# Kernel optimization log

Hardware: AMD Instinct MI355X
Metric: run time of the kernel (lower is better)

The kernel has to match this reference:

```python
import jax, jax.numpy as jnp
import numpy as np

# Fixed-point fake-quant config: Q8.8 (int_bits=8, frac_bits=8, 16-bit signed total)
INT_BITS = 8
FRAC_BITS = 8
SCALE = 2.0 ** FRAC_BITS
QMIN = float(-(2 ** (INT_BITS + FRAC_BITS - 1)))
QMAX = float(2 ** (INT_BITS + FRAC_BITS - 1) - 1)


def fpq(x):
    # round-to-nearest, clamp to signed Q8.8 range, rescale; straight-through estimator
    q = jnp.clip(jnp.round(x * SCALE), QMIN, QMAX) / SCALE
    return x + jax.lax.stop_gradient(q - x)


def qconv2d(x, w, b):
    # stride 1, padding 1, 3x3 kernel -> SAME spatial size
    y = jax.lax.conv_general_dilated(
        x, w, window_strides=(1, 1), padding=((1, 1), (1, 1)),
        dimension_numbers=("NCHW", "OIHW", "NCHW"))
    return fpq(y + b[None, :, None, None])


def qmaxpool2(x):
    y = jax.lax.reduce_window(x, -jnp.inf, jax.lax.max,
                              window_dimensions=(1, 1, 2, 2),
                              window_strides=(1, 1, 2, 2), padding="VALID")
    return fpq(y)


def qlinear(x, w, b):
    return fpq(x @ w.T + b)


def setup_inputs() -> dict:
    key = jax.random.key(0)
    ks = jax.random.split(key, 9)
    B = 4096
    x = jax.random.normal(ks[0], (B, 1, 28, 28), dtype=jnp.float32)
    conv1_w = jax.random.normal(ks[1], (16, 1, 3, 3), dtype=jnp.float32) * 0.1
    conv1_b = jax.random.normal(ks[2], (16,), dtype=jnp.float32) * 0.01
    conv2_w = jax.random.normal(ks[3], (32, 16, 3, 3), dtype=jnp.float32) * 0.05
    conv2_b = jax.random.normal(ks[4], (32,), dtype=jnp.float32) * 0.01
    fc1_w = jax.random.normal(ks[5], (128, 32 * 7 * 7), dtype=jnp.float32) * 0.02
    fc1_b = jax.random.normal(ks[6], (128,), dtype=jnp.float32) * 0.01
    fc2_w = jax.random.normal(ks[7], (10, 128), dtype=jnp.float32) * 0.05
    fc2_b = jax.random.normal(ks[8], (10,), dtype=jnp.float32) * 0.01
    return {"x": x, "conv1_w": conv1_w, "conv1_b": conv1_b,
            "conv2_w": conv2_w, "conv2_b": conv2_b,
            "fc1_w": fc1_w, "fc1_b": fc1_b, "fc2_w": fc2_w, "fc2_b": fc2_b}


def reference(x, conv1_w, conv1_b, conv2_w, conv2_b, fc1_w, fc1_b, fc2_w, fc2_b):
    h = jax.nn.relu(qconv2d(x, conv1_w, conv1_b))          # [B,16,28,28]
    h = qmaxpool2(h)                                        # [B,16,14,14]
    h = jax.nn.relu(qconv2d(h, conv2_w, conv2_b))          # [B,32,14,14]
    h = qmaxpool2(h)                                        # [B,32,7,7]
    h = h.reshape(h.shape[0], 32 * 7 * 7)
    h = jax.nn.relu(qlinear(h, fc1_w, fc1_b))              # [B,128]
    return qlinear(h, fc2_w, fc2_b)                        # [B,10]
```

## Files before the change

kernel.cpp:

```cpp
#include <hip/hip_runtime.h>

typedef _Float16 half4 __attribute__((ext_vector_type(4)));
typedef float f32x4 __attribute__((ext_vector_type(4)));

__global__ void prep_kernel(const float* __restrict__ w1, const float* __restrict__ b1,
                            const float* __restrict__ w2, const float* __restrict__ b2,
                            const float* __restrict__ f1w, const float* __restrict__ f1b,
                            _Float16* __restrict__ wsB, _Float16* __restrict__ wsF,
                            float* __restrict__ w1s, float* __restrict__ b1s,
                            float* __restrict__ b2s, float* __restrict__ b1fs) {
    int i = blockIdx.x * 256 + threadIdx.x;
    if (i < 144) w1s[i]  = __fmul_rn(w1[i], 256.0f);
    if (i < 16)  b1s[i]  = __fmul_rn(b1[i], 256.0f);
    if (i < 32)  b2s[i]  = __fmul_rn(b2[i], 256.0f);
    if (i < 128) b1fs[i] = __fmul_rn(f1b[i], 256.0f);
    if (i < 9216) {
        int ntile = i / 4608, r = i - ntile * 4608;
        int tap = r / 512;  int r2 = r - tap * 512;
        int split = r2 / 256; int lidx = r2 - split * 256;
        int lane = lidx >> 2, j = lidx & 3;
        int ic = ((lane >> 4) << 2) + j;
        int oc = ntile * 16 + (lane & 15);
        float w = w2[oc * 144 + ic * 9 + tap];
        _Float16 wh = (_Float16)w;
        wsB[i] = split ? (_Float16)(w - (float)wh) : wh;
    }
    if (i < 401408) {
        int c = i / 4096, rem = i - c * 4096;
        int sp = rem / 2048; int r2 = rem - sp * 2048;
        int nt = r2 / 256; int lidx = r2 - nt * 256;
        int lane = lidx >> 2, j = lidx & 3;
        int k = c * 16 + ((lane >> 4) << 2) + j;
        int o = nt * 16 + (lane & 15);
        float w = f1w[(size_t)o * 1568 + k];
        _Float16 wh = (_Float16)w;
        wsF[i] = sp ? (_Float16)(w - (float)wh) : wh;
    }
}

#define ICGS 1168

__global__ __launch_bounds__(256) void conv_kernel(
    const float* __restrict__ x,
    const float* __restrict__ w1s, const float* __restrict__ b1s,
    const _Float16* __restrict__ wsB, const float* __restrict__ b2s,
    short* __restrict__ h2s)
{
    __shared__ __align__(16) float    xs[900];
    __shared__ __align__(16) _Float16 h1h[4 * ICGS];
    __shared__ __align__(16) short    c2s[6272];

    const int t = threadIdx.x;
    const int s = blockIdx.x;
    const int lane = t & 63;
    const int wid = t >> 6;

    for (int i = t; i < 900; i += 256) xs[i] = 0.0f;
    for (int i = t; i < 4 * ICGS; i += 256) h1h[i] = (_Float16)0.0f;
    __syncthreads();

    const float* xin = x + (size_t)s * 784;
    for (int i = t; i < 784; i += 256) {
        int r = i / 28, c = i - r * 28;
        xs[(r + 1) * 30 + c + 1] = xin[i];
    }
    __syncthreads();

    {
        const int p  = (t < 196) ? t : 195;
        const int py = p / 14, px = p - 14 * (p / 14);
        const int r0 = 2 * py, c0 = 2 * px;
        float patch[16];
        #pragma unroll
        for (int i = 0; i < 4; ++i)
            #pragma unroll
            for (int j = 0; j < 4; ++j)
                patch[i * 4 + j] = xs[(r0 + i) * 30 + c0 + j];
        #pragma unroll 1
        for (int oc = 0; oc < 16; ++oc) {
            float a0 = 0.f, a1 = 0.f, a2 = 0.f, a3 = 0.f;
            #pragma unroll
            for (int ky = 0; ky < 3; ++ky)
                #pragma unroll
                for (int kx = 0; kx < 3; ++kx) {
                    float w = w1s[oc * 9 + ky * 3 + kx];
                    a0 = __fmaf_rn(patch[ky * 4 + kx],           w, a0);
                    a1 = __fmaf_rn(patch[ky * 4 + kx + 1],       w, a1);
                    a2 = __fmaf_rn(patch[(ky + 1) * 4 + kx],     w, a2);
                    a3 = __fmaf_rn(patch[(ky + 1) * 4 + kx + 1], w, a3);
                }
            float bb = b1s[oc];
            float q0 = rintf(__fadd_rn(a0, bb));
            float q1 = rintf(__fadd_rn(a1, bb));
            float q2 = rintf(__fadd_rn(a2, bb));
            float q3 = rintf(__fadd_rn(a3, bb));
            float m = fmaxf(fmaxf(fmaxf(q0, q1), fmaxf(q2, q3)), 0.f);
            if (t < 196)
                h1h[(oc >> 2) * ICGS + ((py + 1) * 18 + (px + 1)) * 4 + (oc & 3)] = (_Float16)m;
        }
    }
    __syncthreads();

    const half4* __restrict__ wsB4 = (const half4*)wsB;
    for (int nt = 0; nt < 2; ++nt) {
        half4 bh[9], bl[9];
        #pragma unroll
        for (int tap = 0; tap < 9; ++tap) {
            bh[tap] = wsB4[(size_t)((nt * 9 + tap) * 2 + 0) * 64 + lane];
            bl[tap] = wsB4[(size_t)((nt * 9 + tap) * 2 + 1) * 64 + lane];
        }
        const float bb = b2s[nt * 16 + (lane & 15)];
        for (int mt = wid; mt < 13; mt += 4) {
            int p = mt * 16 + (lane & 15);
            p = (p < 196) ? p : 195;
            const int y = p / 14, xx = p - 14 * (p / 14);
            const _Float16* abase = h1h + (lane >> 4) * ICGS + (y * 18 + xx) * 4;

            f32x4 acc = {0.f, 0.f, 0.f, 0.f};
            #pragma unroll
            for (int tap = 0; tap < 9; ++tap) {
                const int aoff = ((tap / 3) * 18 + (tap % 3)) * 4;
                half4 a = *(const half4*)(abase + aoff);
                acc = __builtin_amdgcn_mfma_f32_16x16x16f16(a, bh[tap], acc, 0, 0, 0);
                acc = __builtin_amdgcn_mfma_f32_16x16x16f16(a, bl[tap], acc, 0, 0, 0);
            }
            const int oc = nt * 16 + (lane & 15);
            const int pix0 = mt * 16 + (lane >> 4) * 4;
            #pragma unroll
            for (int j = 0; j < 4; ++j) {
                float qv = fmaxf(rintf(__fadd_rn(acc[j], bb)), 0.f);
                int pix = pix0 + j;
                if (pix < 196) c2s[oc * 196 + pix] = (short)(int)qv;
            }
        }
    }
    __syncthreads();

    short* h2o = h2s + (size_t)s * 1568;
    for (int i = t; i < 1568; i += 256) {
        int oc = i / 49, q = i - oc * 49;
        int qy = q / 7, qx = q - 7 * (q / 7);
        const short* b = c2s + oc * 196 + qy * 28 + qx * 2;
        int m = max(max((int)b[0], (int)b[1]), max((int)b[14], (int)b[15]));
        h2o[i] = (short)m;
    }
}

__global__ __launch_bounds__(256) void fc_kernel(
    const short* __restrict__ h2s,
    const _Float16* __restrict__ wsF, const float* __restrict__ b1fs,
    const float* __restrict__ w2f, const float* __restrict__ b2f,
    float* __restrict__ out)
{
    __shared__ __align__(16) _Float16 Ash[16 * 393 * 4];
    __shared__ short Fsm[16 * 132];

    const int t = threadIdx.x;
    const int s0 = blockIdx.x * 16;
    const int lane = t & 63;
    const int wid = t >> 6;

    for (int i = t; i < 3136; i += 256) {
        int r = i / 196, c = i - r * 196;
        int4 v = *(const int4*)(h2s + (size_t)(s0 + r) * 1568 + c * 8);
        half4 lo, hi;
        lo[0] = (_Float16)(float)(short)(v.x & 0xffff); lo[1] = (_Float16)(float)(short)(v.x >> 16);
        lo[2] = (_Float16)(float)(short)(v.y & 0xffff); lo[3] = (_Float16)(float)(short)(v.y >> 16);
        hi[0] = (_Float16)(float)(short)(v.z & 0xffff); hi[1] = (_Float16)(float)(short)(v.z >> 16);
        hi[2] = (_Float16)(float)(short)(v.w & 0xffff); hi[3] = (_Float16)(float)(short)(v.w >> 16);
        *(half4*)(Ash + (r * 393 + c * 2) * 4)     = lo;
        *(half4*)(Ash + (r * 393 + c * 2 + 1) * 4) = hi;
    }
    __syncthreads();

    const int nt0 = wid * 2, nt1 = wid * 2 + 1;
    const half4* __restrict__ wsF4 = (const half4*)wsF;
    f32x4 acc0 = {0.f, 0.f, 0.f, 0.f};
    f32x4 acc1 = {0.f, 0.f, 0.f, 0.f};

    for (int c = 0; c < 98; ++c) {
        const int kg = c * 4 + (lane >> 4);
        half4 a = *(const half4*)(Ash + ((lane & 15) * 393 + kg) * 4);
        const size_t base = (size_t)(c * 2) * 512 + lane;
        half4 b0h = wsF4[base + (size_t)nt0 * 64];
        half4 b0l = wsF4[base + 512 + (size_t)nt0 * 64];
        half4 b1h = wsF4[base + (size_t)nt1 * 64];
        half4 b1l = wsF4[base + 512 + (size_t)nt1 * 64];
        acc0 = __builtin_amdgcn_mfma_f32_16x16x16f16(a, b0h, acc0, 0, 0, 0);
        acc0 = __builtin_amdgcn_mfma_f32_16x16x16f16(a, b0l, acc0, 0, 0, 0);
        acc1 = __builtin_amdgcn_mfma_f32_16x16x16f16(a, b1h, acc1, 0, 0, 0);
        acc1 = __builtin_amdgcn_mfma_f32_16x16x16f16(a, b1l, acc1, 0, 0, 0);
    }

    {
        const float bb0 = b1fs[nt0 * 16 + (lane & 15)];
        const float bb1 = b1fs[nt1 * 16 + (lane & 15)];
        const int rbase = (lane >> 4) * 4;
        #pragma unroll
        for (int j = 0; j < 4; ++j) {
            float q0 = fmaxf(rintf(__fadd_rn(acc0[j], bb0)), 0.f);
            float q1 = fmaxf(rintf(__fadd_rn(acc1[j], bb1)), 0.f);
            Fsm[(rbase + j) * 132 + nt0 * 16 + (lane & 15)] = (short)(int)q0;
            Fsm[(rbase + j) * 132 + nt1 * 16 + (lane & 15)] = (short)(int)q1;
        }
    }
    __syncthreads();

    if (t < 160) {
        int r = t / 10, c = t - 10 * (t / 10);
        const float* wr = w2f + c * 128;
        double acc = 0.0;
        #pragma unroll 8
        for (int k = 0; k < 128; ++k)
            acc = fma((double)Fsm[r * 132 + k], (double)wr[k], acc);
        out[(size_t)(s0 + r) * 10 + c] = (float)(acc * 0.00390625 + (double)b2f[c]);
    }
}

extern "C" void kernel_launch(void* const* d_in, const int* in_sizes, int n_in,
                              void* d_out, int out_size, void* d_ws, size_t ws_size,
                              hipStream_t stream) {
    const float* x   = (const float*)d_in[0];
    const float* c1w = (const float*)d_in[1];
    const float* c1b = (const float*)d_in[2];
    const float* c2w = (const float*)d_in[3];
    const float* c2b = (const float*)d_in[4];
    const float* f1w = (const float*)d_in[5];
    const float* f1b = (const float*)d_in[6];
    const float* f2w = (const float*)d_in[7];
    const float* f2b = (const float*)d_in[8];
    float* out = (float*)d_out;

    const int B = in_sizes[0] / 784;

    _Float16* wsB = (_Float16*)d_ws;
    _Float16* wsF = wsB + 9216;
    float* fbase  = (float*)(wsF + 401408);
    float* w1s  = fbase;
    float* b1s  = w1s + 144;
    float* b2s  = b1s + 16;
    float* b1fs = b2s + 32;
    short* h2s  = (short*)(b1fs + 128);

    prep_kernel<<<1568, 256, 0, stream>>>(c1w, c1b, c2w, c2b, f1w, f1b,
                                          wsB, wsF, w1s, b1s, b2s, b1fs);
    conv_kernel<<<B, 256, 0, stream>>>(x, w1s, b1s, wsB, b2s, h2s);
    fc_kernel<<<B / 16, 256, 0, stream>>>(h2s, wsF, b1fs, f2w, f2b, out);
}
```

Measured before the change: 82.26 us.

## Split FC into per-N-tile fc1 and separate fc2; fold horizontal pooling into conv epilogue

The conv kernel now max-pools horizontally in the MFMA epilogue, writing a half-size LDS buffer that is unioned with the input tile, and stores pooled activations as fp16. The single fc kernel is split in two. In fc1, each block handles one 16-column output tile, each wave covers 16 samples, and the A operand is read directly from global memory without LDS staging. fc2 is a separate per-output kernel running in double precision. The aim is more parallelism in the FC stage, less LDS use and lower occupancy pressure in conv, and no per-block conversion pass. In exchange it adds a kernel launch and an intermediate global buffer, and fc1 re-reads activations once per N tile.

```diff
diff --git a/kernel.cpp b/kernel.cpp
--- a/kernel.cpp
+++ b/kernel.cpp
@@ -44,25 +44,27 @@
     const float* __restrict__ x,
     const float* __restrict__ w1s, const float* __restrict__ b1s,
     const _Float16* __restrict__ wsB, const float* __restrict__ b2s,
-    short* __restrict__ h2s)
+    _Float16* __restrict__ h2h)
 {
-    __shared__ __align__(16) float    xs[900];
+    __shared__ __align__(16) union {
+        float xs[900];
+        short c2h[32 * 98];
+    } u;
     __shared__ __align__(16) _Float16 h1h[4 * ICGS];
-    __shared__ __align__(16) short    c2s[6272];
 
     const int t = threadIdx.x;
     const int s = blockIdx.x;
     const int lane = t & 63;
     const int wid = t >> 6;
 
-    for (int i = t; i < 900; i += 256) xs[i] = 0.0f;
+    for (int i = t; i < 900; i += 256) u.xs[i] = 0.0f;
     for (int i = t; i < 4 * ICGS; i += 256) h1h[i] = (_Float16)0.0f;
     __syncthreads();
 
     const float* xin = x + (size_t)s * 784;
     for (int i = t; i < 784; i += 256) {
         int r = i / 28, c = i - r * 28;
-        xs[(r + 1) * 30 + c + 1] = xin[i];
+        u.xs[(r + 1) * 30 + c + 1] = xin[i];
     }
     __syncthreads();
 
@@ -75,7 +77,7 @@
         for (int i = 0; i < 4; ++i)
             #pragma unroll
             for (int j = 0; j < 4; ++j)
-                patch[i * 4 + j] = xs[(r0 + i) * 30 + c0 + j];
+                patch[i * 4 + j] = u.xs[(r0 + i) * 30 + c0 + j];
         #pragma unroll 1
         for (int oc = 0; oc < 16; ++oc) {
             float a0 = 0.f, a1 = 0.f, a2 = 0.f, a3 = 0.f;
@@ -126,95 +128,78 @@
             }
             const int oc = nt * 16 + (lane & 15);
             const int pix0 = mt * 16 + (lane >> 4) * 4;
-            #pragma unroll
-            for (int j = 0; j < 4; ++j) {
-                float qv = fmaxf(rintf(__fadd_rn(acc[j], bb)), 0.f);
-                int pix = pix0 + j;
-                if (pix < 196) c2s[oc * 196 + pix] = (short)(int)qv;
+            if (pix0 < 196) {
+                float q0 = fmaxf(rintf(__fadd_rn(acc[0], bb)), 0.f);
+                float q1 = fmaxf(rintf(__fadd_rn(acc[1], bb)), 0.f);
+                float q2 = fmaxf(rintf(__fadd_rn(acc[2], bb)), 0.f);
+                float q3 = fmaxf(rintf(__fadd_rn(acc[3], bb)), 0.f);
+                float h01 = fmaxf(q0, q1);
+                float h23 = fmaxf(q2, q3);
+                int p2 = pix0 + 2;
+                u.c2h[oc * 98 + (pix0 / 14) * 7 + ((pix0 % 14) >> 1)] = (short)(int)h01;
+                u.c2h[oc * 98 + (p2   / 14) * 7 + ((p2   % 14) >> 1)] = (short)(int)h23;
             }
         }
     }
     __syncthreads();
 
-    short* h2o = h2s + (size_t)s * 1568;
+    _Float16* h2o = h2h + (size_t)s * 1568;
     for (int i = t; i < 1568; i += 256) {
         int oc = i / 49, q = i - oc * 49;
         int qy = q / 7, qx = q - 7 * (q / 7);
-        const short* b = c2s + oc * 196 + qy * 28 + qx * 2;
-        int m = max(max((int)b[0], (int)b[1]), max((int)b[14], (int)b[15]));
-        h2o[i] = (short)m;
-    }
-}
-
-__global__ __launch_bounds__(256) void fc_kernel(
-    const short* __restrict__ h2s,
-    const _Float16* __restrict__ wsF, const float* __restrict__ b1fs,
-    const float* __restrict__ w2f, const float* __restrict__ b2f,
-    float* __restrict__ out)
+        int m = max((int)u.c2h[oc * 98 + (2 * qy) * 7 + qx],
+                    (int)u.c2h[oc * 98 + (2 * qy + 1) * 7 + qx]);
+        h2o[i] = (_Float16)(float)m;
+    }
+}
+
+__global__ __launch_bounds__(256) void fc1_kernel(
+    const _Float16* __restrict__ h2h, const _Float16* __restrict__ wsF,
+    const float* __restrict__ b1fs, short* __restrict__ F16)
 {
-    __shared__ __align__(16) _Float16 Ash[16 * 393 * 4];
-    __shared__ short Fsm[16 * 132];
-
     const int t = threadIdx.x;
-    const int s0 = blockIdx.x * 16;
     const int lane = t & 63;
     const int wid = t >> 6;
-
-    for (int i = t; i < 3136; i += 256) {
-        int r = i / 196, c = i - r * 196;
-        int4 v = *(const int4*)(h2s + (size_t)(s0 + r) * 1568 + c * 8);
-        half4 lo, hi;
-        lo[0] = (_Float16)(float)(short)(v.x & 0xffff); lo[1] = (_Float16)(float)(short)(v.x >> 16);
-        lo[2] = (_Float16)(float)(short)(v.y & 0xffff); lo[3] = (_Float16)(float)(short)(v.y >> 16);
-        hi[0] = (_Float16)(float)(short)(v.z & 0xffff); hi[1] = (_Float16)(float)(short)(v.z >> 16);
-        hi[2] = (_Float16)(float)(short)(v.w & 0xffff); hi[3] = (_Float16)(float)(short)(v.w >> 16);
-        *(half4*)(Ash + (r * 393 + c * 2) * 4)     = lo;
-        *(half4*)(Ash + (r * 393 + c * 2 + 1) * 4) = hi;
-    }
-    __syncthreads();
-
-    const int nt0 = wid * 2, nt1 = wid * 2 + 1;
+    const int nt = blockIdx.x & 7;
+    const int s0 = ((blockIdx.x >> 3) * 4 + wid) * 16;
+
     const half4* __restrict__ wsF4 = (const half4*)wsF;
-    f32x4 acc0 = {0.f, 0.f, 0.f, 0.f};
-    f32x4 acc1 = {0.f, 0.f, 0.f, 0.f};
-
+    const _Float16* __restrict__ abase =
+        h2h + (size_t)(s0 + (lane & 15)) * 1568 + (lane >> 4) * 4;
+
+    f32x4 acc = {0.f, 0.f, 0.f, 0.f};
     for (int c = 0; c < 98; ++c) {
-        const int kg = c * 4 + (lane >> 4);
-        half4 a = *(const half4*)(Ash + ((lane & 15) * 393 + kg) * 4);
-        const size_t base = (size_t)(c * 2) * 512 + lane;
-        half4 b0h = wsF4[base + (size_t)nt0 * 64];
-        half4 b0l = wsF4[base + 512 + (size_t)nt0 * 64];
-        half4 b1h = wsF4[base + (size_t)nt1 * 64];
-        half4 b1l = wsF4[base + 512 + (size_t)nt1 * 64];
-        acc0 = __builtin_amdgcn_mfma_f32_16x16x16f16(a, b0h, acc0, 0, 0, 0);
-        acc0 = __builtin_amdgcn_mfma_f32_16x16x16f16(a, b0l, acc0, 0, 0, 0);
-        acc1 = __builtin_amdgcn_mfma_f32_16x16x16f16(a, b1h, acc1, 0, 0, 0);
-        acc1 = __builtin_amdgcn_mfma_f32_16x16x16f16(a, b1l, acc1, 0, 0, 0);
-    }
-
-    {
-        const float bb0 = b1fs[nt0 * 16 + (lane & 15)];
-        const float bb1 = b1fs[nt1 * 16 + (lane & 15)];
-        const int rbase = (lane >> 4) * 4;
-        #pragma unroll
-        for (int j = 0; j < 4; ++j) {
-            float q0 = fmaxf(rintf(__fadd_rn(acc0[j], bb0)), 0.f);
-            float q1 = fmaxf(rintf(__fadd_rn(acc1[j], bb1)), 0.f);
-            Fsm[(rbase + j) * 132 + nt0 * 16 + (lane & 15)] = (short)(int)q0;
-            Fsm[(rbase + j) * 132 + nt1 * 16 + (lane & 15)] = (short)(int)q1;
-        }
-    }
-    __syncthreads();
-
-    if (t < 160) {
-        int r = t / 10, c = t - 10 * (t / 10);
-        const float* wr = w2f + c * 128;
-        double acc = 0.0;
-        #pragma unroll 8
-        for (int k = 0; k < 128; ++k)
-            acc = fma((double)Fsm[r * 132 + k], (double)wr[k], acc);
-        out[(size_t)(s0 + r) * 10 + c] = (float)(acc * 0.00390625 + (double)b2f[c]);
-    }
+        half4 a = *(const half4*)(abase + c * 16);
+        const size_t base = (size_t)(c * 2) * 512 + (size_t)nt * 64 + lane;
+        half4 bh = wsF4[base];
+        half4 bl = wsF4[base + 512];
+        acc = __builtin_amdgcn_mfma_f32_16x16x16f16(a, bh, acc, 0, 0, 0);
+        acc = __builtin_amdgcn_mfma_f32_16x16x16f16(a, bl, acc, 0, 0, 0);
+    }
+    const int o = nt * 16 + (lane & 15);
+    const float bb = b1fs[o];
+    #pragma unroll
+    for (int j = 0; j < 4; ++j) {
+        int smp = s0 + (lane >> 4) * 4 + j;
+        float qv = fmaxf(rintf(__fadd_rn(acc[j], bb)), 0.f);
+        F16[(size_t)smp * 128 + o] = (short)(int)qv;
+    }
+}
+
+__global__ __launch_bounds__(256) void fc2_kernel(
+    const short* __restrict__ F16, const float* __restrict__ w2f,
+    const float* __restrict__ b2f, float* __restrict__ out, int n)
+{
+    int idx = blockIdx.x * 256 + threadIdx.x;
+    if (idx >= n) return;
+    int s = idx / 10, c = idx - 10 * (idx / 10);
+    const short* Fr = F16 + (size_t)s * 128;
+    const float* wr = w2f + c * 128;
+    double acc = 0.0;
+    #pragma unroll 8
+    for (int k = 0; k < 128; ++k)
+        acc = fma((double)Fr[k], (double)wr[k], acc);
+    out[idx] = (float)(acc * 0.00390625 + (double)b2f[c]);
 }
 
 extern "C" void kernel_launch(void* const* d_in, const int* in_sizes, int n_in,
@@ -240,10 +225,12 @@
     float* b1s  = w1s + 144;
     float* b2s  = b1s + 16;
     float* b1fs = b2s + 32;
-    short* h2s  = (short*)(b1fs + 128);
+    _Float16* h2h = (_Float16*)(b1fs + 128);
+    short* F16  = (short*)(h2h + (size_t)B * 1568);
 
     prep_kernel<<<1568, 256, 0, stream>>>(c1w, c1b, c2w, c2b, f1w, f1b,
                                           wsB, wsF, w1s, b1s, b2s, b1fs);
-    conv_kernel<<<B, 256, 0, stream>>>(x, w1s, b1s, wsB, b2s, h2s);
-    fc_kernel<<<B / 16, 256, 0, stream>>>(h2s, wsF, b1fs, f2w, f2b, out);
-}
+    conv_kernel<<<B, 256, 0, stream>>>(x, w1s, b1s, wsB, b2s, h2h);
+    fc1_kernel<<<(B / 64) * 8, 256, 0, stream>>>(h2h, wsF, b1fs, F16);
+    fc2_kernel<<<(B * 10 + 255) / 256, 256, 0, stream>>>(F16, f2w, f2b, out, B * 10);
+}
```

Result: slower. 91.55 us (+11.3%).
